# Kernel tuning notes

Measured on AMD Instinct MI355X. Metric: run time of the kernel, lower is better.

The kernel has to match this reference:

```python
import jax, jax.numpy as jnp
import numpy as np

N = 50000; E = 800000; IN = 128; OUT = 64; ED = 16; H = 4
NEG_SLOPE = 0.2


def adaptive_avg_pool1d(v, L):
    """torch F.adaptive_avg_pool1d on a 1-D vector v -> length L (static slices)."""
    S = v.shape[0]
    return jnp.stack([v[(i * S) // L: -((-(i + 1) * S) // L)].mean() for i in range(L)])


def gat_conv(x, edge_index, edge_attr, W_gat, att_src, att_dst, W_edge, att_edge, b_gat):
    """PyG GATConv(heads=H, concat=False, edge_dim=ED), eval mode (no dropout)."""
    n = x.shape[0]
    h, c = att_src.shape
    xs = (x @ W_gat).reshape(n, h, c)                       # [N,H,C]
    a_src = jnp.einsum('nhc,hc->nh', xs, att_src)           # [N,H]
    a_dst = jnp.einsum('nhc,hc->nh', xs, att_dst)           # [N,H]
    e = (edge_attr @ W_edge).reshape(-1, h, c)              # [E,H,C]
    a_edge = jnp.einsum('ehc,hc->eh', e, att_edge)          # [E,H]
    src, dst = edge_index[0], edge_index[1]
    alpha = a_src[src] + a_dst[dst] + a_edge                # [E,H]
    alpha = jax.nn.leaky_relu(alpha, NEG_SLOPE)
    # segment softmax over incoming edges of each destination node
    amax = jax.ops.segment_max(alpha, dst, num_segments=n)  # [N,H]
    ex = jnp.exp(alpha - amax[dst])
    denom = jax.ops.segment_sum(ex, dst, num_segments=n)
    alpha = ex / (denom[dst] + 1e-16)
    msg = xs[src] * alpha[:, :, None]                       # [E,H,C]
    out = jax.ops.segment_sum(msg, dst, num_segments=n)     # [N,H,C]
    return out.mean(axis=1) + b_gat                         # concat=False -> head mean


def setup_inputs():
    key = jax.random.key(0)
    ks = jax.random.split(key, 16)
    p = lambda k, s: jax.random.normal(k, s, dtype=jnp.float32) * 0.05
    return {
        'x': jax.random.normal(ks[0], (N, IN), dtype=jnp.float32),
        'edge_index': jax.random.randint(ks[1], (2, E), 0, N),
        'edge_attr': jax.random.normal(ks[2], (E, ED), dtype=jnp.float32),
        'quality_raw': jax.random.uniform(ks[3], (E, 4), dtype=jnp.float32),
        'network_state': jax.random.uniform(ks[4], (8,), dtype=jnp.float32),
        'W_gat': p(ks[5], (IN, H * OUT)),
        'att_src': p(ks[6], (H, OUT)),
        'att_dst': p(ks[7], (H, OUT)),
        'W_edge': p(ks[8], (ED, H * OUT)),
        'att_edge': p(ks[9], (H, OUT)),
        'b_gat': jnp.zeros((OUT,), jnp.float32),
        'W_q1': p(ks[10], (4, ED // 2)),
        'b_q1': jnp.zeros((ED // 2,), jnp.float32),
        'W_q2': p(ks[11], (ED // 2, ED)),
        'b_q2': jnp.zeros((ED,), jnp.float32),
        'W_c': p(ks[12], (OUT + ED, OUT)),
        'b_c': jnp.zeros((OUT,), jnp.float32),
    }


def reference(x, edge_index, edge_attr, quality_raw, network_state,
              W_gat, att_src, att_dst, W_edge, att_edge, b_gat,
              W_q1, b_q1, W_q2, b_q2, W_c, b_c):
    # vectorized path-quality encoder (replaces per-edge python loop)
    q = jax.nn.relu(quality_raw @ W_q1 + b_q1) @ W_q2 + b_q2      # [E,ED]
    enhanced_edge_attr = edge_attr + q
    x_conv = gat_conv(x, edge_index, enhanced_edge_attr,
                      W_gat, att_src, att_dst, W_edge, att_edge, b_gat)  # [N,OUT]
    cf = adaptive_avg_pool1d(network_state, ED)                    # [ED]
    cf = jnp.broadcast_to(cf, (x.shape[0], ED))                    # [N,ED]
    h = jnp.concatenate([x_conv, cf], axis=-1)                     # [N,OUT+ED]
    return jax.nn.relu(h @ W_c + b_c)                              # [N,OUT]
```

## Files before the change

kernel.cpp:

```cpp
#include <hip/hip_runtime.h>
#include <hip/hip_bf16.h>

#define NN 50000
#define EE 800000
#define NEG 0.2f
#define NS (NN*8)
#define NSB 391
#define NGB 1563
#define NDB 782

using u32 = unsigned int;
typedef short short4v __attribute__((ext_vector_type(4)));
typedef float f32x4 __attribute__((ext_vector_type(4)));

__device__ __forceinline__ unsigned short f2bf(float f){
  u32 b = __float_as_uint(f);
  b += 0x7FFFu + ((b >> 16) & 1u);
  return (unsigned short)(b >> 16);
}

__global__ __launch_bounds__(256) void k_pre_all(
        const float* __restrict__ Wg, const float* __restrict__ W_c,
        const float* __restrict__ W_edge, const float* __restrict__ att_edge,
        const float* __restrict__ b_c, const float* __restrict__ ns,
        const float* __restrict__ b_gat,
        const float* __restrict__ att_src, const float* __restrict__ att_dst,
        unsigned short* __restrict__ WzB, float* __restrict__ Wt,
        float* __restrict__ cvec, uint2* __restrict__ avp){
  int bid = blockIdx.x, tid = threadIdx.x;
  if (bid < 128){
    __shared__ float sWg[256];
    __shared__ float sWc[64*64];
    sWg[tid] = Wg[bid*256 + tid];
    for (int i = tid; i < 4096; i += 256) sWc[i] = W_c[i];
    __syncthreads();
    int h = tid >> 6, j = tid & 63;
    float s = 0.f;
    #pragma unroll 8
    for (int c = 0; c < 64; c++) s += sWg[h*64 + c] * sWc[c*64 + j];
    int t = tid >> 4, lr = tid & 15;
    int ks = bid >> 4, lg = (bid >> 2) & 3, q = bid & 3;
    int l = lg*16 + lr;
    WzB[(((t*8 + ks)*64 + l) << 2) + q] = f2bf(s);
  } else if (bid == 128){
    if (tid < 64){
      int d = tid >> 2, h = tid & 3;
      float s = 0.f;
      for (int c = 0; c < 64; c++) s += W_edge[d*256 + h*64 + c] * att_edge[h*64 + c];
      Wt[d*4 + h] = s;
    } else if (tid < 128){
      int j = tid - 64;
      float s = b_c[j];
      for (int d = 0; d < 16; d++) s += ns[d >> 1] * W_c[(64 + d)*64 + j];
      for (int c = 0; c < 64; c++) s += b_gat[c] * W_c[c*64 + j];
      cvec[j] = s;
    }
  } else {
    __shared__ float sav2[1024];
    for (int i = tid; i < 1024; i += 256){
      int k = i >> 3, o = i & 7, h = o & 3;
      const float* att = (o < 4) ? att_src : att_dst;
      float s = 0.f;
      for (int c = 0; c < 64; c++) s += Wg[k*256 + h*64 + c] * att[h*64 + c];
      sav2[i] = s;
    }
    __syncthreads();
    if (tid < 64){
      int l = tid, lg = l >> 4, lr = l & 15;
      for (int ks = 0; ks < 8; ks++){
        unsigned int h0, h1, h2, h3;
        int kb = ks*16 + lg*4;
        h0 = (lr < 8) ? f2bf(sav2[(kb+0)*8 + lr]) : 0u;
        h1 = (lr < 8) ? f2bf(sav2[(kb+1)*8 + lr]) : 0u;
        h2 = (lr < 8) ? f2bf(sav2[(kb+2)*8 + lr]) : 0u;
        h3 = (lr < 8) ? f2bf(sav2[(kb+3)*8 + lr]) : 0u;
        uint2 u; u.x = h0 | (h1 << 16); u.y = h2 | (h3 << 16);
        avp[ks*64 + l] = u;
      }
    }
  }
}

__global__ __launch_bounds__(256) void k_main(const float* __restrict__ x,
        const unsigned short* __restrict__ WzB, const uint2* __restrict__ avp,
        const int* __restrict__ dsts,
        __hip_bfloat16* __restrict__ zs,
        float* __restrict__ a_src, float* __restrict__ a_dst,
        u32* __restrict__ deg8, unsigned short* __restrict__ rank){
  __shared__ alignas(16) __hip_bfloat16 zt[4][16][136];
  int tid = threadIdx.x;
  int bid = blockIdx.x;

  if (bid >= NGB){
    int g = bid - NGB;
    int gi = g*256 + tid;
    if (gi*4 < EE){
      int shard = g & 7;
      u32* dg = deg8 + (size_t)shard*NN;
      int4 d4 = *(const int4*)(dsts + (size_t)gi*4);
      u32 r0 = atomicAdd(&dg[d4.x], 1u);
      u32 r1 = atomicAdd(&dg[d4.y], 1u);
      u32 r2 = atomicAdd(&dg[d4.z], 1u);
      u32 r3 = atomicAdd(&dg[d4.w], 1u);
      uint2 pk;
      pk.x = (r0 & 0xffffu) | (r1 << 16);
      pk.y = (r2 & 0xffffu) | (r3 << 16);
      *(uint2*)(rank + (size_t)gi*4) = pk;
    }
    return;
  }

  int w = tid >> 6, l = tid & 63;
  int lr = l & 15, lg = l >> 4;
  int rw = w >> 1, ch = w & 1;
  int n0 = bid*32 + rw*16;

  short4v afr[8];
  #pragma unroll
  for (int ks = 0; ks < 8; ks++){
    int row = n0 + lr; if (row >= NN) row = NN - 1;
    float4 xa = *(const float4*)(x + (size_t)row*128 + ks*16 + lg*4);
    short4v a;
    a[0] = (short)f2bf(xa.x); a[1] = (short)f2bf(xa.y);
    a[2] = (short)f2bf(xa.z); a[3] = (short)f2bf(xa.w);
    afr[ks] = a;
  }
  if (ch == 0){
    f32x4 cad = {0.f, 0.f, 0.f, 0.f};
    #pragma unroll
    for (int ks = 0; ks < 8; ks++){
      short4v b = __builtin_bit_cast(short4v, avp[ks*64 + l]);
      cad = __builtin_amdgcn_mfma_f32_16x16x16bf16_1k(afr[ks], b, cad, 0, 0, 0);
    }
    #pragma unroll
    for (int r = 0; r < 4; r++){
      int n = n0 + lg*4 + r;
      if (n < NN){
        if (lr < 4)      a_src[(size_t)n*4 + lr]       = cad[r];
        else if (lr < 8) a_dst[(size_t)n*4 + (lr - 4)] = cad[r];
      }
    }
  }

  #pragma unroll 4
  for (int t8 = 0; t8 < 8; t8++){
    int t = ch*8 + t8;
    f32x4 c = {0.f, 0.f, 0.f, 0.f};
    #pragma unroll
    for (int ks = 0; ks < 8; ks++){
      short4v b = *(const short4v*)(WzB + (((t*8 + ks)*64 + l) << 2));
      c = __builtin_amdgcn_mfma_f32_16x16x16bf16_1k(afr[ks], b, c, 0, 0, 0);
    }
    #pragma unroll
    for (int r = 0; r < 4; r++)
      zt[w][lg*4 + r][t8*16 + lr] = __float2bfloat16(c[r]);
  }
  #pragma unroll
  for (int i = 0; i < 4; i++){
    int f = i*64 + l;
    int row = f >> 4, c16 = f & 15;
    int n = n0 + row;
    if (n < NN)
      *(uint4*)(zs + (size_t)n*256 + ch*128 + c16*8) = *(const uint4*)&zt[w][row][c16*8];
  }
}

__global__ __launch_bounds__(1024) void k_scan1(const u32* __restrict__ deg8,
                                                u32* __restrict__ offs8, u32* __restrict__ bsum){
  __shared__ u32 sd[1024];
  int t = threadIdx.x;
  int i = blockIdx.x*1024 + t;
  u32 v = (i < NS) ? deg8[(size_t)(i & 7)*NN + (i >> 3)] : 0u;
  sd[t] = v; __syncthreads();
  for (int off = 1; off < 1024; off <<= 1){
    u32 u = (t >= off) ? sd[t-off] : 0u;
    __syncthreads();
    sd[t] += u;
    __syncthreads();
  }
  if (i < NS) offs8[i] = sd[t] - v;
  if (t == 1023) bsum[blockIdx.x] = sd[1023];
}

__global__ __launch_bounds__(1024) void k_scan2(u32* __restrict__ offs8,
                                                const u32* __restrict__ bsum){
  __shared__ u32 sd[1024];
  int b = blockIdx.x, t = threadIdx.x;
  sd[t] = (t < b) ? bsum[t] : 0u;
  __syncthreads();
  #pragma unroll
  for (int off = 512; off; off >>= 1){
    if (t < off) sd[t] += sd[t + off];
    __syncthreads();
  }
  u32 p = sd[0];
  int i = b*1024 + t;
  if (i < NS) offs8[i] += p;
  if (b == 0 && t == 0) offs8[NS] = EE;
}

__global__ __launch_bounds__(256) void k_edge(const float* __restrict__ qraw,
        const float* __restrict__ eattr, const int* __restrict__ eidx,
        const float* __restrict__ Wq1, const float* __restrict__ bq1,
        const float* __restrict__ Wq2, const float* __restrict__ bq2,
        const float* __restrict__ Wt,
        const float* __restrict__ a_src, const float* __restrict__ a_dst,
        const u32* __restrict__ offs8, const unsigned short* __restrict__ rank,
        uint4* __restrict__ csr){
  __shared__ float sWq1[32], sbq1[8], sWq2[128], sbq2[16], sWt[64];
  int tid = threadIdx.x;
  if (tid < 32) sWq1[tid] = Wq1[tid];
  else if (tid < 40)  sbq1[tid-32]  = bq1[tid-32];
  else if (tid < 168) sWq2[tid-40]  = Wq2[tid-40];
  else if (tid < 184) sbq2[tid-168] = bq2[tid-168];
  else if (tid < 248) sWt[tid-184]  = Wt[tid-184];
  __syncthreads();
  int e = blockIdx.x*256 + tid;
  if (e >= EE) return;
  int shard = (blockIdx.x >> 2) & 7;

  float4 qr = *(const float4*)(qraw + (size_t)e*4);
  float t1[8];
  #pragma unroll
  for (int j = 0; j < 8; j++){
    float s = sbq1[j] + qr.x*sWq1[j] + qr.y*sWq1[8+j] + qr.z*sWq1[16+j] + qr.w*sWq1[24+j];
    t1[j] = fmaxf(s, 0.f);
  }
  float ae[4] = {0.f,0.f,0.f,0.f};
  const float* ea = eattr + (size_t)e*16;
  #pragma unroll
  for (int d = 0; d < 16; d++){
    float q = sbq2[d];
    #pragma unroll
    for (int j = 0; j < 8; j++) q += t1[j]*sWq2[j*16 + d];
    float v = ea[d] + q;
    #pragma unroll
    for (int h = 0; h < 4; h++) ae[h] += v * sWt[d*4 + h];
  }
  int src = eidx[e], dst = eidx[EE + e];
  float4 as4 = *(const float4*)(a_src + (size_t)src*4);
  float4 ad4 = *(const float4*)(a_dst + (size_t)dst*4);
  float av4[4] = {as4.x + ad4.x + ae[0], as4.y + ad4.y + ae[1],
                  as4.z + ad4.z + ae[2], as4.w + ad4.w + ae[3]};
  u32 pk[4];
  #pragma unroll
  for (int hh = 0; hh < 4; hh++){
    float a = av4[hh];
    a = (a >= 0.f) ? a : NEG*a;
    pk[hh] = (u32)f2bf(a);
  }
  u32 pos = offs8[(size_t)dst*8 + shard] + (u32)rank[e];
  uint4 q;
  q.x = (u32)src;
  q.y = pk[0] | (pk[1] << 16);
  q.z = pk[2] | (pk[3] << 16);
  q.w = 0u;
  csr[pos] = q;
}

__global__ __launch_bounds__(256) void k_agg(const __hip_bfloat16* __restrict__ zs,
        const uint4* __restrict__ csr, const u32* __restrict__ offs8,
        const float* __restrict__ cvec, float* __restrict__ out){
  int tid = threadIdx.x;
  int w = tid >> 6, lane = tid & 63;
  int n = blockIdx.x*4 + w;
  int h = lane >> 4;
  u32 p0 = offs8[(size_t)n*8], p1 = offs8[(size_t)n*8 + 8];
  float d = 0.f;
  float a0 = 0.f, a1 = 0.f, a2 = 0.f, a3 = 0.f;
  u32 p = p0;
  for (; p + 4 <= p1; p += 4){
    uint4 q0 = csr[p+0], q1 = csr[p+1], q2 = csr[p+2], q3 = csr[p+3];
    u32 w0p = (h < 2) ? q0.y : q0.z,  w1p = (h < 2) ? q1.y : q1.z;
    u32 w2p = (h < 2) ? q2.y : q2.z,  w3p = (h < 2) ? q3.y : q3.z;
    int sh = (h & 1) ? 0 : 16;
    float al0 = __uint_as_float((w0p << sh) & 0xffff0000u);
    float al1 = __uint_as_float((w1p << sh) & 0xffff0000u);
    float al2 = __uint_as_float((w2p << sh) & 0xffff0000u);
    float al3 = __uint_as_float((w3p << sh) & 0xffff0000u);
    uint2 v0 = *(const uint2*)(zs + (size_t)q0.x*256 + lane*4);
    uint2 v1 = *(const uint2*)(zs + (size_t)q1.x*256 + lane*4);
    uint2 v2 = *(const uint2*)(zs + (size_t)q2.x*256 + lane*4);
    uint2 v3 = *(const uint2*)(zs + (size_t)q3.x*256 + lane*4);
    float w0 = __expf(al0), w1 = __expf(al1), w2 = __expf(al2), w3 = __expf(al3);
    a0 += w0*__uint_as_float(v0.x << 16)        + w1*__uint_as_float(v1.x << 16)
        + w2*__uint_as_float(v2.x << 16)        + w3*__uint_as_float(v3.x << 16);
    a1 += w0*__uint_as_float(v0.x & 0xffff0000u)+ w1*__uint_as_float(v1.x & 0xffff0000u)
        + w2*__uint_as_float(v2.x & 0xffff0000u)+ w3*__uint_as_float(v3.x & 0xffff0000u);
    a2 += w0*__uint_as_float(v0.y << 16)        + w1*__uint_as_float(v1.y << 16)
        + w2*__uint_as_float(v2.y << 16)        + w3*__uint_as_float(v3.y << 16);
    a3 += w0*__uint_as_float(v0.y & 0xffff0000u)+ w1*__uint_as_float(v1.y & 0xffff0000u)
        + w2*__uint_as_float(v2.y & 0xffff0000u)+ w3*__uint_as_float(v3.y & 0xffff0000u);
    d  += (w0 + w1) + (w2 + w3);
  }
  for (; p < p1; p++){
    uint4 q0 = csr[p];
    u32 w0p = (h < 2) ? q0.y : q0.z;
    int sh = (h & 1) ? 0 : 16;
    float al = __uint_as_float((w0p << sh) & 0xffff0000u);
    uint2 v0 = *(const uint2*)(zs + (size_t)q0.x*256 + lane*4);
    float w0 = __expf(al);
    a0 += w0*__uint_as_float(v0.x << 16);
    a1 += w0*__uint_as_float(v0.x & 0xffff0000u);
    a2 += w0*__uint_as_float(v0.y << 16);
    a3 += w0*__uint_as_float(v0.y & 0xffff0000u);
    d  += w0;
  }
  float inv = (d > 0.f) ? 0.25f / d : 0.f;
  a0 *= inv; a1 *= inv; a2 *= inv; a3 *= inv;
  a0 += __shfl_xor(a0, 16); a1 += __shfl_xor(a1, 16);
  a2 += __shfl_xor(a2, 16); a3 += __shfl_xor(a3, 16);
  a0 += __shfl_xor(a0, 32); a1 += __shfl_xor(a1, 32);
  a2 += __shfl_xor(a2, 32); a3 += __shfl_xor(a3, 32);
  if (lane < 16){
    float4 cv = *(const float4*)(cvec + lane*4);
    float4 o4;
    o4.x = fmaxf(a0 + cv.x, 0.f);
    o4.y = fmaxf(a1 + cv.y, 0.f);
    o4.z = fmaxf(a2 + cv.z, 0.f);
    o4.w = fmaxf(a3 + cv.w, 0.f);
    *(float4*)(out + (size_t)n*64 + lane*4) = o4;
  }
}

extern "C" void kernel_launch(void* const* d_in, const int* in_sizes, int n_in,
                              void* d_out, int out_size, void* d_ws, size_t ws_size,
                              hipStream_t stream){
  const float* x       = (const float*)d_in[0];
  const int*   eidx    = (const int*)d_in[1];
  const float* eattr   = (const float*)d_in[2];
  const float* qraw    = (const float*)d_in[3];
  const float* ns      = (const float*)d_in[4];
  const float* Wg      = (const float*)d_in[5];
  const float* att_src = (const float*)d_in[6];
  const float* att_dst = (const float*)d_in[7];
  const float* W_edge  = (const float*)d_in[8];
  const float* att_edge= (const float*)d_in[9];
  const float* b_gat   = (const float*)d_in[10];
  const float* Wq1     = (const float*)d_in[11];
  const float* bq1     = (const float*)d_in[12];
  const float* Wq2     = (const float*)d_in[13];
  const float* bq2     = (const float*)d_in[14];
  const float* W_c     = (const float*)d_in[15];
  const float* b_c     = (const float*)d_in[16];
  float* out = (float*)d_out;

  char* ws = (char*)d_ws;
  __hip_bfloat16* zs = (__hip_bfloat16*)ws;
  uint4* csr      = (uint4*)(ws + 25600000);
  u32* deg8       = (u32*)(ws + 25600000);
  u32* offs8      = (u32*)(ws + 38400000);
  float* a_src    = (float*)(ws + 40000064);
  float* a_dst    = (float*)(ws + 40800064);
  unsigned short* rank = (unsigned short*)(ws + 41600064);
  u32* bsum       = (u32*)(ws + 43200064);
  unsigned short* WzB = (unsigned short*)(ws + 43202112);
  uint2* avp      = (uint2*)(ws + 43267648);
  float* Wt       = (float*)(ws + 43271744);
  float* cvec     = (float*)(ws + 43272000);

  hipMemsetAsync(deg8, 0, (size_t)NN*8*4, stream);

  k_pre_all<<<130,      256, 0, stream>>>(Wg, W_c, W_edge, att_edge, b_c, ns, b_gat,
                                          att_src, att_dst, WzB, Wt, cvec, avp);
  k_main   <<<NGB+NDB,  256, 0, stream>>>(x, WzB, avp, eidx + EE, zs, a_src, a_dst,
                                          deg8, rank);
  k_scan1  <<<NSB,     1024, 0, stream>>>(deg8, offs8, bsum);
  k_scan2  <<<NSB,     1024, 0, stream>>>(offs8, bsum);
  k_edge   <<<3125,     256, 0, stream>>>(qraw, eattr, eidx, Wq1, bq1, Wq2, bq2, Wt,
                                          a_src, a_dst, offs8, rank, csr);
  k_agg    <<<12500,    256, 0, stream>>>(zs, csr, offs8, cvec, out);
}
```

Baseline: 179.2 us.

## Use 16 interleaved degree shards, split CSR arrays, stage x via LDS, interleave blocks

Degree counters go from 8 planar shards to 16 shards interleaved per node, so a node's counters are contiguous and contention per counter drops. The scan then reads them sequentially, but it processes twice as many entries. The 16-byte CSR record becomes a 4-byte source array plus an 8-byte alpha array, cutting edge-list bytes in k_edge and k_agg. k_main now stages x rows through LDS with coalesced loads and interleaves degree-counting blocks with GEMM blocks (every third block) so atomics overlap with MFMA work.

```diff
diff --git a/kernel.cpp b/kernel.cpp
--- a/kernel.cpp
+++ b/kernel.cpp
@@ -4,8 +4,9 @@
 #define NN 50000
 #define EE 800000
 #define NEG 0.2f
-#define NS (NN*8)
-#define NSB 391
+#define NSH 16
+#define NS (NN*NSH)
+#define NSB 782
 #define NGB 1563
 #define NDB 782
 
@@ -86,22 +87,21 @@
         const int* __restrict__ dsts,
         __hip_bfloat16* __restrict__ zs,
         float* __restrict__ a_src, float* __restrict__ a_dst,
-        u32* __restrict__ deg8, unsigned short* __restrict__ rank){
-  __shared__ alignas(16) __hip_bfloat16 zt[4][16][136];
+        u32* __restrict__ deg16, unsigned short* __restrict__ rank){
+  __shared__ alignas(16) char ldsu[17408];
   int tid = threadIdx.x;
   int bid = blockIdx.x;
 
-  if (bid >= NGB){
-    int g = bid - NGB;
+  if ((bid % 3) == 1){
+    int g = bid / 3;
     int gi = g*256 + tid;
     if (gi*4 < EE){
-      int shard = g & 7;
-      u32* dg = deg8 + (size_t)shard*NN;
+      int shard = g & (NSH-1);
       int4 d4 = *(const int4*)(dsts + (size_t)gi*4);
-      u32 r0 = atomicAdd(&dg[d4.x], 1u);
-      u32 r1 = atomicAdd(&dg[d4.y], 1u);
-      u32 r2 = atomicAdd(&dg[d4.z], 1u);
-      u32 r3 = atomicAdd(&dg[d4.w], 1u);
+      u32 r0 = atomicAdd(&deg16[((size_t)(u32)d4.x << 4) | shard], 1u);
+      u32 r1 = atomicAdd(&deg16[((size_t)(u32)d4.y << 4) | shard], 1u);
+      u32 r2 = atomicAdd(&deg16[((size_t)(u32)d4.z << 4) | shard], 1u);
+      u32 r3 = atomicAdd(&deg16[((size_t)(u32)d4.w << 4) | shard], 1u);
       uint2 pk;
       pk.x = (r0 & 0xffffu) | (r1 << 16);
       pk.y = (r2 & 0xffffu) | (r3 << 16);
@@ -110,16 +110,37 @@
     return;
   }
 
+  int gb = bid - (bid + 2)/3;
   int w = tid >> 6, l = tid & 63;
   int lr = l & 15, lg = l >> 4;
   int rw = w >> 1, ch = w & 1;
-  int n0 = bid*32 + rw*16;
+  int nb = gb*32;
+  int n0 = nb + rw*16;
+
+  float* xsl = (float*)ldsu;
+  __hip_bfloat16* ztp = (__hip_bfloat16*)ldsu;
+
+  {
+    float4 stg[4];
+    #pragma unroll
+    for (int i = 0; i < 4; i++){
+      int s = w*256 + i*64 + l;
+      int r = s >> 5, c = s & 31;
+      int row = nb + r; if (row >= NN) row = NN - 1;
+      stg[i] = *(const float4*)(x + (size_t)row*128 + c*4);
+    }
+    #pragma unroll
+    for (int i = 0; i < 4; i++){
+      int s = w*256 + i*64 + l;
+      *(float4*)(xsl + s*4) = stg[i];
+    }
+  }
+  __syncthreads();
 
   short4v afr[8];
   #pragma unroll
   for (int ks = 0; ks < 8; ks++){
-    int row = n0 + lr; if (row >= NN) row = NN - 1;
-    float4 xa = *(const float4*)(x + (size_t)row*128 + ks*16 + lg*4);
+    float4 xa = *(const float4*)(xsl + ((rw*16 + lr)*128 + ks*16 + lg*4));
     short4v a;
     a[0] = (short)f2bf(xa.x); a[1] = (short)f2bf(xa.y);
     a[2] = (short)f2bf(xa.z); a[3] = (short)f2bf(xa.w);
@@ -141,6 +162,7 @@
       }
     }
   }
+  __syncthreads();
 
   #pragma unroll 4
   for (int t8 = 0; t8 < 8; t8++){
@@ -153,7 +175,7 @@
     }
     #pragma unroll
     for (int r = 0; r < 4; r++)
-      zt[w][lg*4 + r][t8*16 + lr] = __float2bfloat16(c[r]);
+      ztp[((w*16) + lg*4 + r)*136 + t8*16 + lr] = __float2bfloat16(c[r]);
   }
   #pragma unroll
   for (int i = 0; i < 4; i++){
@@ -161,16 +183,16 @@
     int row = f >> 4, c16 = f & 15;
     int n = n0 + row;
     if (n < NN)
-      *(uint4*)(zs + (size_t)n*256 + ch*128 + c16*8) = *(const uint4*)&zt[w][row][c16*8];
-  }
-}
-
-__global__ __launch_bounds__(1024) void k_scan1(const u32* __restrict__ deg8,
-                                                u32* __restrict__ offs8, u32* __restrict__ bsum){
+      *(uint4*)(zs + (size_t)n*256 + ch*128 + c16*8) = *(const uint4*)&ztp[(w*16 + row)*136 + c16*8];
+  }
+}
+
+__global__ __launch_bounds__(1024) void k_scan1(const u32* __restrict__ deg16,
+                                                u32* __restrict__ offs16, u32* __restrict__ bsum){
   __shared__ u32 sd[1024];
   int t = threadIdx.x;
   int i = blockIdx.x*1024 + t;
-  u32 v = (i < NS) ? deg8[(size_t)(i & 7)*NN + (i >> 3)] : 0u;
+  u32 v = (i < NS) ? deg16[i] : 0u;
   sd[t] = v; __syncthreads();
   for (int off = 1; off < 1024; off <<= 1){
     u32 u = (t >= off) ? sd[t-off] : 0u;
@@ -178,11 +200,11 @@
     sd[t] += u;
     __syncthreads();
   }
-  if (i < NS) offs8[i] = sd[t] - v;
+  if (i < NS) offs16[i] = sd[t] - v;
   if (t == 1023) bsum[blockIdx.x] = sd[1023];
 }
 
-__global__ __launch_bounds__(1024) void k_scan2(u32* __restrict__ offs8,
+__global__ __launch_bounds__(1024) void k_scan2(u32* __restrict__ offs16,
                                                 const u32* __restrict__ bsum){
   __shared__ u32 sd[1024];
   int b = blockIdx.x, t = threadIdx.x;
@@ -195,8 +217,8 @@
   }
   u32 p = sd[0];
   int i = b*1024 + t;
-  if (i < NS) offs8[i] += p;
-  if (b == 0 && t == 0) offs8[NS] = EE;
+  if (i < NS) offs16[i] += p;
+  if (b == 0 && t == 0) offs16[NS] = EE;
 }
 
 __global__ __launch_bounds__(256) void k_edge(const float* __restrict__ qraw,
@@ -205,8 +227,8 @@
         const float* __restrict__ Wq2, const float* __restrict__ bq2,
         const float* __restrict__ Wt,
         const float* __restrict__ a_src, const float* __restrict__ a_dst,
-        const u32* __restrict__ offs8, const unsigned short* __restrict__ rank,
-        uint4* __restrict__ csr){
+        const u32* __restrict__ offs16, const unsigned short* __restrict__ rank,
+        u32* __restrict__ srcs, uint2* __restrict__ al8){
   __shared__ float sWq1[32], sbq1[8], sWq2[128], sbq2[16], sWt[64];
   int tid = threadIdx.x;
   if (tid < 32) sWq1[tid] = Wq1[tid];
@@ -217,7 +239,7 @@
   __syncthreads();
   int e = blockIdx.x*256 + tid;
   if (e >= EE) return;
-  int shard = (blockIdx.x >> 2) & 7;
+  int shard = (blockIdx.x >> 2) & (NSH-1);
 
   float4 qr = *(const float4*)(qraw + (size_t)e*4);
   float t1[8];
@@ -249,39 +271,40 @@
     a = (a >= 0.f) ? a : NEG*a;
     pk[hh] = (u32)f2bf(a);
   }
-  u32 pos = offs8[(size_t)dst*8 + shard] + (u32)rank[e];
-  uint4 q;
-  q.x = (u32)src;
-  q.y = pk[0] | (pk[1] << 16);
-  q.z = pk[2] | (pk[3] << 16);
-  q.w = 0u;
-  csr[pos] = q;
+  u32 pos = offs16[((size_t)(u32)dst << 4) | shard] + (u32)rank[e];
+  srcs[pos] = (u32)src;
+  uint2 q;
+  q.x = pk[0] | (pk[1] << 16);
+  q.y = pk[2] | (pk[3] << 16);
+  al8[pos] = q;
 }
 
 __global__ __launch_bounds__(256) void k_agg(const __hip_bfloat16* __restrict__ zs,
-        const uint4* __restrict__ csr, const u32* __restrict__ offs8,
+        const u32* __restrict__ srcs, const uint2* __restrict__ al8,
+        const u32* __restrict__ offs16,
         const float* __restrict__ cvec, float* __restrict__ out){
   int tid = threadIdx.x;
   int w = tid >> 6, lane = tid & 63;
   int n = blockIdx.x*4 + w;
   int h = lane >> 4;
-  u32 p0 = offs8[(size_t)n*8], p1 = offs8[(size_t)n*8 + 8];
+  u32 p0 = offs16[(size_t)n << 4], p1 = offs16[((size_t)n << 4) + 16];
   float d = 0.f;
   float a0 = 0.f, a1 = 0.f, a2 = 0.f, a3 = 0.f;
+  int sh = (h & 1) ? 0 : 16;
   u32 p = p0;
   for (; p + 4 <= p1; p += 4){
-    uint4 q0 = csr[p+0], q1 = csr[p+1], q2 = csr[p+2], q3 = csr[p+3];
-    u32 w0p = (h < 2) ? q0.y : q0.z,  w1p = (h < 2) ? q1.y : q1.z;
-    u32 w2p = (h < 2) ? q2.y : q2.z,  w3p = (h < 2) ? q3.y : q3.z;
-    int sh = (h & 1) ? 0 : 16;
+    u32 s0 = srcs[p+0], s1 = srcs[p+1], s2 = srcs[p+2], s3 = srcs[p+3];
+    uint2 q0 = al8[p+0], q1 = al8[p+1], q2 = al8[p+2], q3 = al8[p+3];
+    u32 w0p = (h < 2) ? q0.x : q0.y,  w1p = (h < 2) ? q1.x : q1.y;
+    u32 w2p = (h < 2) ? q2.x : q2.y,  w3p = (h < 2) ? q3.x : q3.y;
     float al0 = __uint_as_float((w0p << sh) & 0xffff0000u);
     float al1 = __uint_as_float((w1p << sh) & 0xffff0000u);
     float al2 = __uint_as_float((w2p << sh) & 0xffff0000u);
     float al3 = __uint_as_float((w3p << sh) & 0xffff0000u);
-    uint2 v0 = *(const uint2*)(zs + (size_t)q0.x*256 + lane*4);
-    uint2 v1 = *(const uint2*)(zs + (size_t)q1.x*256 + lane*4);
-    uint2 v2 = *(const uint2*)(zs + (size_t)q2.x*256 + lane*4);
-    uint2 v3 = *(const uint2*)(zs + (size_t)q3.x*256 + lane*4);
+    uint2 v0 = *(const uint2*)(zs + (size_t)s0*256 + lane*4);
+    uint2 v1 = *(const uint2*)(zs + (size_t)s1*256 + lane*4);
+    uint2 v2 = *(const uint2*)(zs + (size_t)s2*256 + lane*4);
+    uint2 v3 = *(const uint2*)(zs + (size_t)s3*256 + lane*4);
     float w0 = __expf(al0), w1 = __expf(al1), w2 = __expf(al2), w3 = __expf(al3);
     a0 += w0*__uint_as_float(v0.x << 16)        + w1*__uint_as_float(v1.x << 16)
         + w2*__uint_as_float(v2.x << 16)        + w3*__uint_as_float(v3.x << 16);
@@ -294,11 +317,11 @@
     d  += (w0 + w1) + (w2 + w3);
   }
   for (; p < p1; p++){
-    uint4 q0 = csr[p];
-    u32 w0p = (h < 2) ? q0.y : q0.z;
-    int sh = (h & 1) ? 0 : 16;
+    u32 s0 = srcs[p];
+    uint2 q0 = al8[p];
+    u32 w0p = (h < 2) ? q0.x : q0.y;
     float al = __uint_as_float((w0p << sh) & 0xffff0000u);
-    uint2 v0 = *(const uint2*)(zs + (size_t)q0.x*256 + lane*4);
+    uint2 v0 = *(const uint2*)(zs + (size_t)s0*256 + lane*4);
     float w0 = __expf(al);
     a0 += w0*__uint_as_float(v0.x << 16);
     a1 += w0*__uint_as_float(v0.x & 0xffff0000u);
@@ -347,27 +370,28 @@
 
   char* ws = (char*)d_ws;
   __hip_bfloat16* zs = (__hip_bfloat16*)ws;
-  uint4* csr      = (uint4*)(ws + 25600000);
-  u32* deg8       = (u32*)(ws + 25600000);
-  u32* offs8      = (u32*)(ws + 38400000);
-  float* a_src    = (float*)(ws + 40000064);
-  float* a_dst    = (float*)(ws + 40800064);
-  unsigned short* rank = (unsigned short*)(ws + 41600064);
-  u32* bsum       = (u32*)(ws + 43200064);
-  unsigned short* WzB = (unsigned short*)(ws + 43202112);
-  uint2* avp      = (uint2*)(ws + 43267648);
-  float* Wt       = (float*)(ws + 43271744);
-  float* cvec     = (float*)(ws + 43272000);
-
-  hipMemsetAsync(deg8, 0, (size_t)NN*8*4, stream);
+  u32* srcs       = (u32*)(ws + 25600000);
+  uint2* al8      = (uint2*)(ws + 28800000);
+  u32* deg16      = (u32*)(ws + 25600000);
+  unsigned short* WzB = (unsigned short*)(ws + 35200000);
+  uint2* avp      = (uint2*)(ws + 35265536);
+  u32* bsum       = (u32*)(ws + 35269632);
+  u32* offs16     = (u32*)(ws + 36000000);
+  float* a_src    = (float*)(ws + 39200064);
+  float* a_dst    = (float*)(ws + 40000064);
+  unsigned short* rank = (unsigned short*)(ws + 40800064);
+  float* Wt       = (float*)(ws + 42400064);
+  float* cvec     = (float*)(ws + 42400320);
+
+  hipMemsetAsync(deg16, 0, (size_t)NS*4, stream);
 
   k_pre_all<<<130,      256, 0, stream>>>(Wg, W_c, W_edge, att_edge, b_c, ns, b_gat,
                                           att_src, att_dst, WzB, Wt, cvec, avp);
   k_main   <<<NGB+NDB,  256, 0, stream>>>(x, WzB, avp, eidx + EE, zs, a_src, a_dst,
-                                          deg8, rank);
-  k_scan1  <<<NSB,     1024, 0, stream>>>(deg8, offs8, bsum);
-  k_scan2  <<<NSB,     1024, 0, stream>>>(offs8, bsum);
+                                          deg16, rank);
+  k_scan1  <<<NSB,     1024, 0, stream>>>(deg16, offs16, bsum);
+  k_scan2  <<<NSB,     1024, 0, stream>>>(offs16, bsum);
   k_edge   <<<3125,     256, 0, stream>>>(qraw, eattr, eidx, Wq1, bq1, Wq2, bq2, Wt,
-                                          a_src, a_dst, offs8, rank, csr);
-  k_agg    <<<12500,    256, 0, stream>>>(zs, csr, offs8, cvec, out);
-}
+                                          a_src, a_dst, offs16, rank, srcs, al8);
+  k_agg    <<<12500,    256, 0, stream>>>(zs, srcs, al8, offs16, cvec, out);
+}
```

Result: slower. 193.5 us (+8.0%).
